# Optimization experiments

Hardware: AMD Instinct MI355X
Metric: run time of the kernel (lower is better)

The kernel has to match this reference:

```python
import jax, jax.numpy as jnp
import numpy as np

F4_MAX = 6.0      # float4 e2m1 max magnitude
F8_MAX = 448.0    # float8 e4m3 max magnitude
BLOCK = 16        # nvfp4 block size along reduction dim


def _fp4_e2m1_rne(v):
    """Round v to the nearest float4 e2m1 value, ties-to-even.
    Representable magnitudes: {0, 0.5, 1, 1.5, 2, 3, 4, 6}."""
    s = jnp.sign(v)
    a = jnp.clip(jnp.abs(v), 0.0, F4_MAX)
    # exponent of the quantization step: subnormals and [1,2) share step 0.5
    e = jnp.clip(jnp.floor(jnp.log2(jnp.maximum(a, 1.0))), 0.0, 2.0)
    step = jnp.exp2(e - 1.0)  # 0.5, 1.0 or 2.0
    q = jnp.round(a / step) * step  # jnp.round is round-half-to-even
    return s * jnp.clip(q, 0.0, F4_MAX)


def _nvfp4_quant_dequant(x, global_scale):
    """scaled_fp4_quant followed by dequant (== what the scaled fp4 GEMM
    with alpha = 1/(gs_a*gs_w) computes per operand)."""
    lead, K = x.shape[:-1], x.shape[-1]
    xb = x.reshape(*lead, K // BLOCK, BLOCK)
    amax = jnp.max(jnp.abs(xb), axis=-1, keepdims=True)            # per-block amax
    scale = (amax * (global_scale / F4_MAX))
    scale = scale.astype(jnp.float8_e4m3fn).astype(jnp.float32)    # e4m3 block scale
    safe = jnp.where(scale > 0.0, scale, 1.0)
    q = _fp4_e2m1_rne(xb * (global_scale / safe))                  # fp4 codes (as floats)
    dq = q * safe / global_scale                                   # dequantized values
    return dq.reshape(x.shape)


def setup_inputs() -> dict:
    key = jax.random.key(0)
    k1, k2, k3 = jax.random.split(key, 3)
    B, S, K, N = 4, 2048, 4096, 4096
    x = jax.random.normal(k1, (B, S, K), dtype=jnp.float32)
    W = jax.random.normal(k2, (N, K), dtype=jnp.float32) * 0.02
    bias = jax.random.normal(k3, (N,), dtype=jnp.float32) * 0.02
    return {"x": x, "W": W, "bias": bias}


def reference(x, W, bias):
    # per-tensor global scales (FLOAT8_E4M3_MAX * FLOAT4_E2M1_MAX / amax)
    x_gs = (F8_MAX * F4_MAX) / jnp.max(jnp.abs(x)).astype(jnp.float32)
    w_gs = (F8_MAX * F4_MAX) / jnp.max(jnp.abs(W)).astype(jnp.float32)
    x_dq = _nvfp4_quant_dequant(x, x_gs)   # [B,S,K]
    w_dq = _nvfp4_quant_dequant(W, w_gs)   # [N,K]
    out = jnp.einsum('bsk,nk->bsn', x_dq, w_dq) + bias
    return out.astype(x.dtype)
```

## Files before the change

kernel.cpp:

```cpp
#include <hip/hip_runtime.h>
#include <stdint.h>

typedef unsigned short u16;
typedef __bf16 bf16x8 __attribute__((ext_vector_type(8)));
typedef float floatx4 __attribute__((ext_vector_type(4)));

__global__ void amax_both_k(const float4* __restrict__ x, long nx4,
                            const float4* __restrict__ w, long nw4,
                            unsigned* slots, int gx) {
    const float4* src; long n4; int bid, nb; unsigned* slot;
    if ((int)blockIdx.x < gx) { src = x; n4 = nx4; bid = blockIdx.x; nb = gx; slot = slots; }
    else { src = w; n4 = nw4; bid = blockIdx.x - gx; nb = gridDim.x - gx; slot = slots + 1; }
    float m = 0.0f;
    long stride = (long)nb * blockDim.x;
    for (long i = (long)bid * blockDim.x + threadIdx.x; i < n4; i += stride) {
        float4 v = src[i];
        m = fmaxf(m, fmaxf(fmaxf(fabsf(v.x), fabsf(v.y)), fmaxf(fabsf(v.z), fabsf(v.w))));
    }
    #pragma unroll
    for (int off = 32; off > 0; off >>= 1)
        m = fmaxf(m, __shfl_down(m, off, 64));
    __shared__ float sm[4];
    int lane = threadIdx.x & 63, wv = threadIdx.x >> 6;
    if (lane == 0) sm[wv] = m;
    __syncthreads();
    if (threadIdx.x == 0) {
        m = fmaxf(fmaxf(sm[0], sm[1]), fmaxf(sm[2], sm[3]));
        atomicMax(slot, __float_as_uint(m));
    }
}

__device__ __forceinline__ float e4m3_rne(float v) {
    unsigned u = __float_as_uint(v);
    u += 0x7FFFFu + ((u >> 20) & 1u);
    float hi = __uint_as_float(u & 0xFFF00000u);
    float lo = rintf(v * 512.0f) * 0.001953125f;
    return (v < 0.015625f) ? lo : hi;
}

__device__ __forceinline__ float fp4_rne(float x) {
    float a = fminf(fabsf(x), 6.0f);
    unsigned u = __float_as_uint(a);
    u += 0x1FFFFFu + ((u >> 22) & 1u);
    float hi = __uint_as_float(u & 0xFFC00000u);
    float lo = rintf(a + a) * 0.5f;
    float q = (a < 1.0f) ? lo : hi;
    return copysignf(q, x);
}

__device__ __forceinline__ unsigned pack2(float d0, float d1) {
    return (__float_as_uint(d0) >> 16) | (__float_as_uint(d1) & 0xFFFF0000u);
}

__global__ void quant_both_k(const float4* __restrict__ x4, const float4* __restrict__ w4,
                             uint2* __restrict__ Aq2, uint2* __restrict__ Bq2,
                             const unsigned* __restrict__ slots, long nx4, long ntot4) {
    float ag0 = __uint_as_float(slots[0]);
    float ag1 = __uint_as_float(slots[1]);
    float gs0 = 2688.0f / ag0, gs1 = 2688.0f / ag1;
    float t0 = gs0 / 6.0f,     t1 = gs1 / 6.0f;
    long stride = (long)gridDim.x * blockDim.x;
    for (long i = (long)blockIdx.x * blockDim.x + threadIdx.x; i < ntot4; i += stride) {
        bool isx = i < nx4;
        float4 v = isx ? x4[i] : w4[i - nx4];
        float gs = isx ? gs0 : gs1;
        float t  = isx ? t0  : t1;
        float am = fmaxf(fmaxf(fabsf(v.x), fabsf(v.y)), fmaxf(fabsf(v.z), fabsf(v.w)));
        am = fmaxf(am, __shfl_xor(am, 1, 4));
        am = fmaxf(am, __shfl_xor(am, 2, 4));
        float sf = e4m3_rne(am * t);
        float r = gs / (sf > 0.0f ? sf : 1.0f);
        uint2 o;
        o.x = pack2(fp4_rne(v.x * r) * sf, fp4_rne(v.y * r) * sf);
        o.y = pack2(fp4_rne(v.z * r) * sf, fp4_rne(v.w * r) * sf);
        if (isx) Aq2[i] = o; else Bq2[i - nx4] = o;
    }
}

#define KTILE 64

#define SFENCE() __builtin_amdgcn_sched_barrier(0)
#define BAR() do { asm volatile("" ::: "memory"); SFENCE(); \
    __builtin_amdgcn_s_barrier(); SFENCE(); asm volatile("" ::: "memory"); } while (0)

#define DSR128O(D, VB, IMM) asm volatile("ds_read_b128 %0, %1 offset:%c2" \
    : "=v"(D) : "v"(VB), "i"(IMM))

#define STAGE_SLOT(GS, LS) do { \
    __builtin_amdgcn_global_load_lds((const __attribute__((address_space(1))) void*)(GS), \
        (__attribute__((address_space(3))) void*)(LS), 16, 0, 0); \
    __builtin_amdgcn_global_load_lds((const __attribute__((address_space(1))) void*)((GS) + row64K), \
        (__attribute__((address_space(3))) void*)((LS) + 4096), 16, 0, 0); \
} while (0)

#define LDA_TO(SET, CURLIT, MH) do { \
    DSR128O(SET[0][0], vA0, ((CURLIT)*32768+(((MH)*64+ 0)*128))); \
    DSR128O(SET[0][1], vA1, ((CURLIT)*32768+(((MH)*64+ 0)*128))); \
    DSR128O(SET[1][0], vA0, ((CURLIT)*32768+(((MH)*64+16)*128))); \
    DSR128O(SET[1][1], vA1, ((CURLIT)*32768+(((MH)*64+16)*128))); \
    DSR128O(SET[2][0], vA0, ((CURLIT)*32768+(((MH)*64+32)*128))); \
    DSR128O(SET[2][1], vA1, ((CURLIT)*32768+(((MH)*64+32)*128))); \
    DSR128O(SET[3][0], vA0, ((CURLIT)*32768+(((MH)*64+48)*128))); \
    DSR128O(SET[3][1], vA1, ((CURLIT)*32768+(((MH)*64+48)*128))); \
} while (0)

#define LDB_TO(SET, CURLIT, NH) do { \
    DSR128O(SET[0][0], vB0, ((CURLIT)*32768+(((NH)*32+ 0)*128))); \
    DSR128O(SET[0][1], vB1, ((CURLIT)*32768+(((NH)*32+ 0)*128))); \
    DSR128O(SET[1][0], vB0, ((CURLIT)*32768+(((NH)*32+16)*128))); \
    DSR128O(SET[1][1], vB1, ((CURLIT)*32768+(((NH)*32+16)*128))); \
} while (0)

#define QUADS(AS, BS, MH, NH) do { \
    _Pragma("unroll") for (int ks = 0; ks < 2; ++ks) \
    _Pragma("unroll") for (int mf = 0; mf < 4; ++mf) \
    _Pragma("unroll") for (int nf = 0; nf < 2; ++nf) \
        acc[(MH)*4+mf][(NH)*2+nf] = __builtin_amdgcn_mfma_f32_16x16x32_bf16( \
            AS[mf][ks], BS[nf][ks], acc[(MH)*4+mf][(NH)*2+nf], 0, 0, 0); \
} while (0)

#define TILE(CUR, NXT, S) do { \
    const u16* gA1 = Ag + (size_t)(((S)+1 < NT) ? (S)+1 : NT-1) * KTILE; \
    const u16* gA2 = Ag + (size_t)(((S)+2 < NT) ? (S)+2 : NT-1) * KTILE; \
    const u16* gB2 = Bg + (size_t)(((S)+2 < NT) ? (S)+2 : NT-1) * KTILE; \
    u16* lA1 = Al + (NXT) * 16384; \
    u16* lA2 = Al + (CUR) * 16384; \
    u16* lB2 = Bl + (CUR) * 16384; \
     \
    LDB_TO(bf_b, CUR, 1); \
    STAGE_SLOT(gA1 + halfGA, lA1 + 8192); \
    BAR(); \
    asm volatile("s_waitcnt lgkmcnt(4)" ::: "memory"); SFENCE(); \
    __builtin_amdgcn_s_setprio(1); QUADS(af_a, bf_a, 0, 0); __builtin_amdgcn_s_setprio(0); \
    BAR(); \
     \
    LDA_TO(af_b, CUR, 1); \
    BAR(); \
    asm volatile("s_waitcnt lgkmcnt(8)" ::: "memory"); SFENCE(); \
    __builtin_amdgcn_s_setprio(1); QUADS(af_a, bf_b, 0, 1); __builtin_amdgcn_s_setprio(0); \
    BAR(); \
     \
    STAGE_SLOT(gB2, lB2); \
    BAR(); \
    asm volatile("s_waitcnt lgkmcnt(0)" ::: "memory"); SFENCE(); \
    __builtin_amdgcn_s_setprio(1); QUADS(af_b, bf_a, 1, 0); __builtin_amdgcn_s_setprio(0); \
    SFENCE(); \
    asm volatile("s_waitcnt vmcnt(2)" ::: "memory"); \
    BAR(); \
     \
    LDA_TO(af_a, NXT, 0); \
    LDB_TO(bf_a, NXT, 0); \
    STAGE_SLOT(gB2 + halfGA, lB2 + 8192); \
    STAGE_SLOT(gA2, lA2); \
    BAR(); \
    __builtin_amdgcn_s_setprio(1); QUADS(af_b, bf_b, 1, 1); __builtin_amdgcn_s_setprio(0); \
    BAR(); \
} while (0)

__global__ __launch_bounds__(512, 2) void gemm_k(
    const u16* __restrict__ A, const u16* __restrict__ B,
    const float* __restrict__ bias, const unsigned* __restrict__ scal,
    float* __restrict__ out, int M, int N, int K)
{
    __shared__ u16 As[2 * 256 * 64];
    __shared__ u16 Bs[2 * 256 * 64];

    const int tid = threadIdx.x;
    const int l   = tid & 63;
    const int wv  = tid >> 6;
    const int wm  = wv >> 2;
    const int wn  = wv & 3;

    const int nTM = M / 256, nTN = N / 256;
    const int nwg = nTM * nTN;
    const int orig = blockIdx.x;
    const int xcd = orig & 7, lid = orig >> 3;
    const int q8 = nwg >> 3, r8 = nwg & 7;
    const int swz = (xcd < r8 ? xcd * (q8 + 1) : r8 * (q8 + 1) + (xcd - r8) * q8) + lid;
    const long tileM = (long)(swz % nTM) * 256;
    const long tileN = (long)(swz / nTM) * 256;

    const int srow  = tid >> 3;
    const int sslot = tid & 7;
    const int schunk = sslot ^ (srow & 7);
    const size_t row64K = (size_t)64 * K;
    const size_t halfGA = (size_t)128 * K;
    const u16* Ag = A + (size_t)(tileM + srow) * K + schunk * 8;
    const u16* Bg = B + (size_t)(tileN + srow) * K + schunk * 8;
    u16* Al = As + wv * 512;
    u16* Bl = Bs + wv * 512;

    const int lr = l & 15;
    const int hi = l >> 4;
    const int ca0 = hi ^ (lr & 7);
    const int ca1 = ca0 ^ 4;
    const unsigned vA0 = (unsigned)(unsigned long long)
        (const __attribute__((address_space(3))) void*)(const void*)(As + (wm * 128 + lr) * 64 + ca0 * 8);
    const unsigned vA1 = (unsigned)(unsigned long long)
        (const __attribute__((address_space(3))) void*)(const void*)(As + (wm * 128 + lr) * 64 + ca1 * 8);
    const unsigned vB0 = (unsigned)(unsigned long long)
        (const __attribute__((address_space(3))) void*)(const void*)(Bs + (wn * 64 + lr) * 64 + ca0 * 8);
    const unsigned vB1 = (unsigned)(unsigned long long)
        (const __attribute__((address_space(3))) void*)(const void*)(Bs + (wn * 64 + lr) * 64 + ca1 * 8);

    floatx4 acc[8][4] = {};
    bf16x8 af_a[4][2], af_b[4][2], bf_a[2][2], bf_b[2][2];

    const int NT = K / KTILE;

    STAGE_SLOT(Bg, Bl);
    STAGE_SLOT(Bg + halfGA, Bl + 8192);
    STAGE_SLOT(Ag, Al);
    STAGE_SLOT(Ag + halfGA, Al + 8192);
    {
        const u16* gB1 = Bg + (size_t)((1 < NT) ? 1 : 0) * KTILE;
        STAGE_SLOT(gB1, Bl + 16384);
        STAGE_SLOT(gB1 + halfGA, Bl + 16384 + 8192);
        const u16* gA1p = Ag + (size_t)((1 < NT) ? 1 : 0) * KTILE;
        STAGE_SLOT(gA1p, Al + 16384);
    }
    SFENCE();
    asm volatile("s_waitcnt vmcnt(6)" ::: "memory");
    BAR();
    LDA_TO(af_a, 0, 0);
    LDB_TO(bf_a, 0, 0);

    for (int s = 0; s < NT; s += 2) {
        TILE(0, 1, s);
        TILE(1, 0, s + 1);
    }

    SFENCE();
    asm volatile("s_waitcnt vmcnt(0) lgkmcnt(0)" ::: "memory");
    SFENCE();

    float ax = __uint_as_float(scal[0]);
    float aw = __uint_as_float(scal[1]);
    float gsx = 2688.0f / ax, gsw = 2688.0f / aw;
    float alpha = 1.0f / (gsx * gsw);

    #pragma unroll
    for (int nq = 0; nq < 4; ++nq) {
        const long col = tileN + wn * 64 + nq * 16 + lr;
        const float bv = bias[col];
        #pragma unroll
        for (int mq = 0; mq < 8; ++mq) {
            const long r0 = tileM + wm * 128 + mq * 16 + hi * 4;
            #pragma unroll
            for (int reg = 0; reg < 4; ++reg)
                out[(size_t)(r0 + reg) * N + col] = acc[mq][nq][reg] * alpha + bv;
        }
    }
}

extern "C" void kernel_launch(void* const* d_in, const int* in_sizes, int n_in,
                              void* d_out, int out_size, void* d_ws, size_t ws_size,
                              hipStream_t stream) {
    const float* x    = (const float*)d_in[0];
    const float* W    = (const float*)d_in[1];
    const float* bias = (const float*)d_in[2];
    float* out = (float*)d_out;

    const int N = in_sizes[2];
    const int K = in_sizes[1] / N;
    const int M = in_sizes[0] / K;

    unsigned* scal = (unsigned*)d_ws;
    u16* Aq = (u16*)((char*)d_ws + 256);
    u16* Bq = Aq + (size_t)M * K;

    hipMemsetAsync(scal, 0, 8, stream);

    const int GX = 2048, GW = 1024;
    hipLaunchKernelGGL(amax_both_k, dim3(GX + GW), dim3(256), 0, stream,
                       (const float4*)x, (long)M * K / 4,
                       (const float4*)W, (long)N * K / 4, scal, GX);

    long nx4 = (long)M * K / 4;
    long nw4 = (long)N * K / 4;
    hipLaunchKernelGGL(quant_both_k, dim3(4096), dim3(256), 0, stream,
                       (const float4*)x, (const float4*)W,
                       (uint2*)Aq, (uint2*)Bq, scal, nx4, nx4 + nw4);

    hipLaunchKernelGGL(gemm_k, dim3((M / 256) * (N / 256)), dim3(512), 0, stream,
                       Aq, Bq, bias, scal, out, M, N, K);
}
```

Measured before the change: 538.1 us.

## Restructure GEMM main loop to load LDS fragments per k-substep within the current tile

Reworks the tile pipeline so that A and B fragments are read from LDS per k-substep inside the current tile, instead of being prefetched from the next buffer at the end of the previous tile. Fine-grained lgkmcnt waits let the first k-substep MFMAs start while the second substep's reads are still in flight. Global-to-LDS staging is rescheduled so A for the next tile is issued at the start of each tile rather than two tiles ahead. The fragment register sets shrink (af/bf instead of two A and two B sets), which lowers VGPR pressure, but the cross-tile LDS prefetch is lost and A prefetch depth is reduced.

```diff
diff --git a/kernel.cpp b/kernel.cpp
--- a/kernel.cpp
+++ b/kernel.cpp
@@ -82,9 +82,10 @@
 #define SFENCE() __builtin_amdgcn_sched_barrier(0)
 #define BAR() do { asm volatile("" ::: "memory"); SFENCE(); \
     __builtin_amdgcn_s_barrier(); SFENCE(); asm volatile("" ::: "memory"); } while (0)
-
-#define DSR128O(D, VB, IMM) asm volatile("ds_read_b128 %0, %1 offset:%c2" \
-    : "=v"(D) : "v"(VB), "i"(IMM))
+#define LGKM(N) do { asm volatile("s_waitcnt lgkmcnt(" #N ")" ::: "memory"); SFENCE(); } while (0)
+
+#define DSR128(D, P) asm volatile("ds_read_b128 %0, %1" : "=v"(D) \
+    : "v"((unsigned)(unsigned long long)(const __attribute__((address_space(3))) void*)(const void*)(P)))
 
 #define STAGE_SLOT(GS, LS) do { \
     __builtin_amdgcn_global_load_lds((const __attribute__((address_space(1))) void*)(GS), \
@@ -93,67 +94,66 @@
         (__attribute__((address_space(3))) void*)((LS) + 4096), 16, 0, 0); \
 } while (0)
 
-#define LDA_TO(SET, CURLIT, MH) do { \
-    DSR128O(SET[0][0], vA0, ((CURLIT)*32768+(((MH)*64+ 0)*128))); \
-    DSR128O(SET[0][1], vA1, ((CURLIT)*32768+(((MH)*64+ 0)*128))); \
-    DSR128O(SET[1][0], vA0, ((CURLIT)*32768+(((MH)*64+16)*128))); \
-    DSR128O(SET[1][1], vA1, ((CURLIT)*32768+(((MH)*64+16)*128))); \
-    DSR128O(SET[2][0], vA0, ((CURLIT)*32768+(((MH)*64+32)*128))); \
-    DSR128O(SET[2][1], vA1, ((CURLIT)*32768+(((MH)*64+32)*128))); \
-    DSR128O(SET[3][0], vA0, ((CURLIT)*32768+(((MH)*64+48)*128))); \
-    DSR128O(SET[3][1], vA1, ((CURLIT)*32768+(((MH)*64+48)*128))); \
-} while (0)
-
-#define LDB_TO(SET, CURLIT, NH) do { \
-    DSR128O(SET[0][0], vB0, ((CURLIT)*32768+(((NH)*32+ 0)*128))); \
-    DSR128O(SET[0][1], vB1, ((CURLIT)*32768+(((NH)*32+ 0)*128))); \
-    DSR128O(SET[1][0], vB0, ((CURLIT)*32768+(((NH)*32+16)*128))); \
-    DSR128O(SET[1][1], vB1, ((CURLIT)*32768+(((NH)*32+16)*128))); \
-} while (0)
-
-#define QUADS(AS, BS, MH, NH) do { \
-    _Pragma("unroll") for (int ks = 0; ks < 2; ++ks) \
+#define LDA_KS(CUR, MH, KS) do { \
+    const int ck_ = (KS) ? ca1 : ca0; \
+    DSR128(af[0][KS], aB + (CUR) * 16384 + (((MH) * 64 +  0) * 64) + ck_ * 8); \
+    DSR128(af[1][KS], aB + (CUR) * 16384 + (((MH) * 64 + 16) * 64) + ck_ * 8); \
+    DSR128(af[2][KS], aB + (CUR) * 16384 + (((MH) * 64 + 32) * 64) + ck_ * 8); \
+    DSR128(af[3][KS], aB + (CUR) * 16384 + (((MH) * 64 + 48) * 64) + ck_ * 8); \
+} while (0)
+
+#define LDB_KS(CUR, NH, KS) do { \
+    const int ck_ = (KS) ? ca1 : ca0; \
+    DSR128(bf[(NH)*2+0][KS], bB + (CUR) * 16384 + (((NH) * 32 +  0) * 64) + ck_ * 8); \
+    DSR128(bf[(NH)*2+1][KS], bB + (CUR) * 16384 + (((NH) * 32 + 16) * 64) + ck_ * 8); \
+} while (0)
+
+#define QUAD_KS(MH, NH, KS) do { \
     _Pragma("unroll") for (int mf = 0; mf < 4; ++mf) \
     _Pragma("unroll") for (int nf = 0; nf < 2; ++nf) \
         acc[(MH)*4+mf][(NH)*2+nf] = __builtin_amdgcn_mfma_f32_16x16x32_bf16( \
-            AS[mf][ks], BS[nf][ks], acc[(MH)*4+mf][(NH)*2+nf], 0, 0, 0); \
-} while (0)
-
-#define TILE(CUR, NXT, S) do { \
+            af[mf][KS], bf[(NH)*2+nf][KS], acc[(MH)*4+mf][(NH)*2+nf], 0, 0, 0); \
+} while (0)
+
+#define TILE(CUR, S) do { \
     const u16* gA1 = Ag + (size_t)(((S)+1 < NT) ? (S)+1 : NT-1) * KTILE; \
-    const u16* gA2 = Ag + (size_t)(((S)+2 < NT) ? (S)+2 : NT-1) * KTILE; \
     const u16* gB2 = Bg + (size_t)(((S)+2 < NT) ? (S)+2 : NT-1) * KTILE; \
-    u16* lA1 = Al + (NXT) * 16384; \
-    u16* lA2 = Al + (CUR) * 16384; \
+    u16* lA1 = Al + ((CUR)^1) * 16384; \
     u16* lB2 = Bl + (CUR) * 16384; \
      \
-    LDB_TO(bf_b, CUR, 1); \
+    LDA_KS(CUR, 0, 0); LDB_KS(CUR, 0, 0); \
+    LDA_KS(CUR, 0, 1); LDB_KS(CUR, 0, 1); \
+    STAGE_SLOT(gA1, lA1); \
+    BAR(); \
+    __builtin_amdgcn_s_setprio(1); \
+    LGKM(6); QUAD_KS(0, 0, 0); \
+    LGKM(0); QUAD_KS(0, 0, 1); \
+    __builtin_amdgcn_s_setprio(0); \
+    BAR(); \
+     \
+    LDB_KS(CUR, 1, 0); LDB_KS(CUR, 1, 1); \
     STAGE_SLOT(gA1 + halfGA, lA1 + 8192); \
     BAR(); \
-    asm volatile("s_waitcnt lgkmcnt(4)" ::: "memory"); SFENCE(); \
-    __builtin_amdgcn_s_setprio(1); QUADS(af_a, bf_a, 0, 0); __builtin_amdgcn_s_setprio(0); \
-    BAR(); \
-     \
-    LDA_TO(af_b, CUR, 1); \
-    BAR(); \
-    asm volatile("s_waitcnt lgkmcnt(8)" ::: "memory"); SFENCE(); \
-    __builtin_amdgcn_s_setprio(1); QUADS(af_a, bf_b, 0, 1); __builtin_amdgcn_s_setprio(0); \
-    BAR(); \
-     \
+    __builtin_amdgcn_s_setprio(1); \
+    LGKM(2); QUAD_KS(0, 1, 0); \
+    LGKM(0); QUAD_KS(0, 1, 1); \
+    __builtin_amdgcn_s_setprio(0); \
+    BAR(); \
+     \
+    LDA_KS(CUR, 1, 0); LDA_KS(CUR, 1, 1); \
     STAGE_SLOT(gB2, lB2); \
     BAR(); \
-    asm volatile("s_waitcnt lgkmcnt(0)" ::: "memory"); SFENCE(); \
-    __builtin_amdgcn_s_setprio(1); QUADS(af_b, bf_a, 1, 0); __builtin_amdgcn_s_setprio(0); \
+    __builtin_amdgcn_s_setprio(1); \
+    LGKM(4); QUAD_KS(1, 0, 0); \
+    LGKM(0); QUAD_KS(1, 0, 1); \
+    __builtin_amdgcn_s_setprio(0); \
+    BAR(); \
+     \
+    STAGE_SLOT(gB2 + halfGA, lB2 + 8192); \
+    BAR(); \
+    __builtin_amdgcn_s_setprio(1); QUAD_KS(1, 1, 0); QUAD_KS(1, 1, 1); __builtin_amdgcn_s_setprio(0); \
     SFENCE(); \
-    asm volatile("s_waitcnt vmcnt(2)" ::: "memory"); \
-    BAR(); \
-     \
-    LDA_TO(af_a, NXT, 0); \
-    LDB_TO(bf_a, NXT, 0); \
-    STAGE_SLOT(gB2 + halfGA, lB2 + 8192); \
-    STAGE_SLOT(gA2, lA2); \
-    BAR(); \
-    __builtin_amdgcn_s_setprio(1); QUADS(af_b, bf_b, 1, 1); __builtin_amdgcn_s_setprio(0); \
+    asm volatile("s_waitcnt vmcnt(4)" ::: "memory"); \
     BAR(); \
 } while (0)
 
@@ -194,17 +194,11 @@
     const int hi = l >> 4;
     const int ca0 = hi ^ (lr & 7);
     const int ca1 = ca0 ^ 4;
-    const unsigned vA0 = (unsigned)(unsigned long long)
-        (const __attribute__((address_space(3))) void*)(const void*)(As + (wm * 128 + lr) * 64 + ca0 * 8);
-    const unsigned vA1 = (unsigned)(unsigned long long)
-        (const __attribute__((address_space(3))) void*)(const void*)(As + (wm * 128 + lr) * 64 + ca1 * 8);
-    const unsigned vB0 = (unsigned)(unsigned long long)
-        (const __attribute__((address_space(3))) void*)(const void*)(Bs + (wn * 64 + lr) * 64 + ca0 * 8);
-    const unsigned vB1 = (unsigned)(unsigned long long)
-        (const __attribute__((address_space(3))) void*)(const void*)(Bs + (wn * 64 + lr) * 64 + ca1 * 8);
+    const u16* aB = As + (wm * 128 + lr) * 64;
+    const u16* bB = Bs + (wn * 64 + lr) * 64;
 
     floatx4 acc[8][4] = {};
-    bf16x8 af_a[4][2], af_b[4][2], bf_a[2][2], bf_b[2][2];
+    bf16x8 af[4][2], bf[4][2];
 
     const int NT = K / KTILE;
 
@@ -213,21 +207,17 @@
     STAGE_SLOT(Ag, Al);
     STAGE_SLOT(Ag + halfGA, Al + 8192);
     {
-        const u16* gB1 = Bg + (size_t)((1 < NT) ? 1 : 0) * KTILE;
+        const u16* gB1 = Bg + ((1 < NT) ? KTILE : 0);
         STAGE_SLOT(gB1, Bl + 16384);
         STAGE_SLOT(gB1 + halfGA, Bl + 16384 + 8192);
-        const u16* gA1p = Ag + (size_t)((1 < NT) ? 1 : 0) * KTILE;
-        STAGE_SLOT(gA1p, Al + 16384);
     }
     SFENCE();
-    asm volatile("s_waitcnt vmcnt(6)" ::: "memory");
+    asm volatile("s_waitcnt vmcnt(4)" ::: "memory");
     BAR();
-    LDA_TO(af_a, 0, 0);
-    LDB_TO(bf_a, 0, 0);
 
     for (int s = 0; s < NT; s += 2) {
-        TILE(0, 1, s);
-        TILE(1, 0, s + 1);
+        TILE(0, s);
+        TILE(1, s + 1);
     }
 
     SFENCE();
```

Result: no change. 535.4 us (-0.5%).
